# Performance work log

Hardware: AMD Instinct MI355X
Metric: run time of the kernel (lower is better)

Reference implementation:

```python
import jax, jax.numpy as jnp
import numpy as np

B, T, N, E = 16, 30, 2048, 32768
F_IN, HID, TEMP, NCLS = 8, 64, 128, 2
EPS = 1e-5  # BatchNorm eps (eval mode, running stats)


def setup_inputs() -> dict:
    key = jax.random.key(0)
    ks = jax.random.split(key, 26)
    def gl(k, shape, fan_in):
        return (jax.random.normal(k, shape, jnp.float32) / np.sqrt(fan_in)).astype(jnp.float32)
    inp = {}
    inp["x"] = jax.random.normal(ks[0], (B, T, N, F_IN), jnp.float32)
    inp["edge_index"] = jax.random.randint(ks[1], (B, T, 2, E), 0, N)
    inp["edge_weight"] = jax.random.uniform(ks[2], (B, T, E), jnp.float32)
    inp["node_ids"] = jax.random.randint(ks[3], (B, T, N), 0, 1000000)
    # GCN layer 1 and 2 (PyG GCNConv: x @ W then normalized aggregation, + bias)
    inp["W1"] = gl(ks[4], (F_IN, HID), F_IN); inp["b1"] = jnp.zeros((HID,), jnp.float32)
    inp["W2"] = gl(ks[5], (HID, HID), HID);   inp["b2"] = jnp.zeros((HID,), jnp.float32)
    # BatchNorm1d params (eval mode with running stats)
    inp["g1"] = jnp.ones((HID,), jnp.float32); inp["be1"] = jnp.zeros((HID,), jnp.float32)
    inp["m1"] = 0.1 * jax.random.normal(ks[6], (HID,), jnp.float32)
    inp["v1"] = jnp.ones((HID,), jnp.float32) + 0.1 * jax.random.uniform(ks[7], (HID,))
    inp["g2"] = jnp.ones((HID,), jnp.float32); inp["be2"] = jnp.zeros((HID,), jnp.float32)
    inp["m2"] = 0.1 * jax.random.normal(ks[8], (HID,), jnp.float32)
    inp["v2"] = jnp.ones((HID,), jnp.float32) + 0.1 * jax.random.uniform(ks[9], (HID,))
    # GRU (PyTorch layout: W_ih [3*TEMP, HID], W_hh [3*TEMP, TEMP])
    inp["Wih"] = gl(ks[10], (3 * TEMP, HID), HID)
    inp["Whh"] = gl(ks[11], (3 * TEMP, TEMP), TEMP)
    inp["bih"] = jnp.zeros((3 * TEMP,), jnp.float32)
    inp["bhh"] = jnp.zeros((3 * TEMP,), jnp.float32)
    # Classifier MLP: TEMP -> TEMP//2 -> NCLS
    inp["Wc1"] = gl(ks[12], (TEMP, TEMP // 2), TEMP); inp["bc1"] = jnp.zeros((TEMP // 2,), jnp.float32)
    inp["Wc2"] = gl(ks[13], (TEMP // 2, NCLS), TEMP // 2); inp["bc2"] = jnp.zeros((NCLS,), jnp.float32)
    return inp


def _gcn(h, src, dst, ew, W, b):
    # PyG GCNConv with self-loops (weight 1) and symmetric normalization.
    hw = h @ W                                     # [N, out]
    deg = jnp.ones((N,), hw.dtype).at[dst].add(ew)  # in-degree incl. self-loop
    dinv = jnp.where(deg > 0, jax.lax.rsqrt(deg), 0.0)
    norm = dinv[src] * ew * dinv[dst]               # [E]
    agg = jnp.zeros_like(hw).at[dst].add(norm[:, None] * hw[src])
    agg = agg + (dinv * dinv)[:, None] * hw         # self-loop contribution
    return agg + b


def _frame(x, ei, ew, nid, W1, b1, g1, be1, m1, v1, W2, b2, g2, be2, m2, v2):
    # node_ids identity alignment: sort rows of x by node_ids
    x = x[jnp.argsort(nid)]
    src, dst = ei[0], ei[1]
    h = _gcn(x, src, dst, ew, W1, b1)
    h = (h - m1) * jax.lax.rsqrt(v1 + EPS) * g1 + be1  # BN eval
    h = jax.nn.relu(h)
    h = _gcn(h, src, dst, ew, W2, b2)
    h = (h - m2) * jax.lax.rsqrt(v2 + EPS) * g2 + be2
    h = jax.nn.relu(h)
    return h.mean(axis=0)  # frame embedding [HID]


def _forward(x, edge_weight, W1, b1, g1, be1, m1, v1, W2, b2, g2, be2, m2, v2,
             Wih, Whh, bih, bhh, Wc1, bc1, Wc2, bc2, edge_index, node_ids):
    G = B * T
    frames = jax.vmap(
        lambda xf, eif, ewf, nidf: _frame(xf, eif, ewf, nidf, W1, b1, g1, be1,
                                          m1, v1, W2, b2, g2, be2, m2, v2)
    )(x.reshape(G, N, F_IN), edge_index.reshape(G, 2, E),
      edge_weight.reshape(G, E), node_ids.reshape(G, N))
    H = frames.reshape(B, T, HID).transpose(1, 0, 2)  # [T, B, HID]

    def gru_step(h, xt):
        gi = xt @ Wih.T + bih
        gh = h @ Whh.T + bhh
        ir, iz, inn = jnp.split(gi, 3, axis=-1)
        hr, hz, hn = jnp.split(gh, 3, axis=-1)
        r = jax.nn.sigmoid(ir + hr)
        z = jax.nn.sigmoid(iz + hz)
        n = jnp.tanh(inn + r * hn)
        return (1.0 - z) * n + z * h, None

    h0 = jnp.zeros((B, TEMP), H.dtype)
    h_final, _ = jax.lax.scan(gru_step, h0, H)
    hidden = jax.nn.relu(h_final @ Wc1 + bc1)
    return hidden @ Wc2 + bc2  # [B, NCLS]


def reference(x, edge_index, edge_weight, node_ids, W1, b1, W2, b2, g1, be1, m1, v1,
              g2, be2, m2, v2, Wih, Whh, bih, bhh, Wc1, bc1, Wc2, bc2):
    return _forward(x, edge_weight, W1, b1, g1, be1, m1, v1, W2, b2, g2, be2, m2, v2,
                    Wih, Whh, bih, bhh, Wc1, bc1, Wc2, bc2, edge_index, node_ids)
```

## Files before the change

kernel.cpp:

```cpp
#include <hip/hip_runtime.h>
#include <hip/hip_fp16.h>
#include <stdint.h>

#define B_   16
#define T_   30
#define NF   480
#define NN   2048
#define EE   32768
#define EPS  1e-5f

typedef unsigned int u32;
typedef unsigned short u16;
typedef __attribute__((ext_vector_type(8))) short short8;
typedef __attribute__((ext_vector_type(4))) float f32x4;

__device__ __forceinline__ u16 f2bf(float f) {
  u32 u = __float_as_uint(f);
  u32 r = u + 0x7FFFu + ((u >> 16) & 1u);
  return (u16)(r >> 16);
}
__device__ __forceinline__ u32 pack2bf(float a, float b) {
  return (u32)f2bf(a) | ((u32)f2bf(b) << 16);
}
__device__ __forceinline__ float bflo(u32 w) { return __uint_as_float(w << 16); }
__device__ __forceinline__ float bfhi(u32 w) { return __uint_as_float(w & 0xFFFF0000u); }
__device__ __forceinline__ u16 f2h(float f) { return __half_as_ushort(__float2half(f)); }
__device__ __forceinline__ float h2f(u16 h) { return __half2float(__ushort_as_half(h)); }
__device__ __forceinline__ u32 pack2h(float a, float b) {
  return (u32)f2h(a) | ((u32)f2h(b) << 16);
}

#define KP_KEYS 0
#define KP_HIST 8192
#define KP_CUM  9216
#define KP_CUR  10240
#define KP_REC  0
#define KP_DINV 131072
#define KP_CNT  139264
#define KP_PERM 147456
#define KP_RANK 151552
#define KP_OFF  155648
#define KP_LDS  156672

__global__ __launch_bounds__(1024) void kPre(
    const int* __restrict__ ei, const float* __restrict__ ew, const int* __restrict__ nid,
    u32* __restrict__ recG, u32* __restrict__ metaG, float* __restrict__ dv2G,
    u32* __restrict__ offG)
{
  extern __shared__ unsigned char smem[];
  const int g = blockIdx.x, t = threadIdx.x;
  const int*   eig  = ei  + (size_t)g * 2 * EE;
  const float* ewg  = ew  + (size_t)g * EE;
  const int*   nidg = nid + (size_t)g * NN;

  u32*  keys = (u32*)(smem + KP_KEYS);
  u32*  hist = (u32*)(smem + KP_HIST);
  u32*  cum  = (u32*)(smem + KP_CUM);
  u32*  cur  = (u32*)(smem + KP_CUR);
  u32*  rec  = (u32*)(smem + KP_REC);
  float* dinv = (float*)(smem + KP_DINV);
  u32*  cnt  = (u32*)(smem + KP_CNT);
  u16*  perm = (u16*)(smem + KP_PERM);
  u16*  rank = (u16*)(smem + KP_RANK);
  u32*  off  = (u32*)(smem + KP_OFF);

  keys[t]        = ((u32)nidg[t] << 11) | (u32)t;
  keys[t + 1024] = ((u32)nidg[t + 1024] << 11) | (u32)(t + 1024);
  dinv[t] = 1.0f; dinv[t + 1024] = 1.0f;
  cnt[t] = 0u; cnt[t + 1024] = 0u;
  __syncthreads();

  for (int k = 2; k <= NN; k <<= 1) {
    for (int j = k >> 1; j > 0; j >>= 1) {
      int i = ((t & ~(j - 1)) << 1) | (t & (j - 1));
      int l = i | j;
      u32 x = keys[i], y = keys[l];
      bool up = ((i & k) == 0);
      if ((x > y) == up) { keys[i] = y; keys[l] = x; }
      __syncthreads();
    }
  }
  perm[2*t]   = (u16)(keys[2*t] & 2047u);
  perm[2*t+1] = (u16)(keys[2*t+1] & 2047u);

  for (int e = t; e < EE; e += 1024) {
    int d = eig[EE + e];
    atomicAdd(&dinv[d], ewg[e]);
    atomicAdd(&cnt[d], 1u);
  }
  __syncthreads();
  dinv[2*t]   = rsqrtf(dinv[2*t]);
  dinv[2*t+1] = rsqrtf(dinv[2*t+1]);

  if (t < 256) hist[t] = 0u;
  __syncthreads();
  for (int i = t; i < NN; i += 1024) {
    u32 L = cnt[i];
    atomicAdd(&hist[L < 255u ? L : 255u], 1u);
  }
  __syncthreads();
  if (t < 256) cum[t] = hist[t];
  __syncthreads();
  for (int o = 1; o < 256; o <<= 1) {
    u32 v = 0u;
    if (t < 256 && t >= o) v = cum[t - o];
    __syncthreads();
    if (t < 256) cum[t] += v;
    __syncthreads();
  }
  if (t < 256) cur[t] = (u32)NN - cum[t];
  __syncthreads();
  if (t < 256) hist[t] = cur[t];
  __syncthreads();
  for (int o = 1; o < 256; o <<= 1) {
    u32 v = 0u;
    if (t < 256 && t >= o) v = hist[t - o];
    __syncthreads();
    if (t < 256) hist[t] += v;
    __syncthreads();
  }
  if (t < 256) {
    u32 ov = hist[t] - cur[t];
    off[t] = ov;
    offG[(size_t)g * 256 + t] = ov;
  }
  __syncthreads();

  for (int i = t; i < NN; i += 1024) {
    u32 L = cnt[i];
    u32 b = L < 255u ? L : 255u;
    u32 r = atomicAdd(&cur[b], 1u);
    rank[i] = (u16)r;
    metaG[(size_t)g * NN + r] = ((u32)perm[i] << 16) | (L & 0xFFFFu);
    float dv = dinv[i];
    dv2G[(size_t)g * NN + r] = dv * dv;
  }
  __syncthreads();
  cnt[t] = 0u; cnt[t + 1024] = 0u;
  __syncthreads();

  for (int e = t; e < EE; e += 1024) {
    int s = eig[e], d = eig[EE + e];
    float nrm = dinv[s] * ewg[e] * dinv[d];
    u32 k = atomicAdd(&cnt[d], 1u);
    u32 pos = off[k] + (u32)rank[d];
    rec[pos] = ((u32)perm[s] << 11) | (u32)(f2h(nrm) >> 5) | ((u32)f2h(nrm) << 27);
    rec[pos] = ((u32)perm[s] << 16) | (u32)f2h(nrm);
  }
  __syncthreads();

  uint4* rg = (uint4*)(recG + (size_t)g * EE);
  const uint4* rl = (const uint4*)rec;
  for (int i = t; i < EE / 4; i += 1024) rg[i] = rl[i];
}

#define KF_H1   0
#define KF_W1   131072
#define KF_T1   133120
#define KF_OFF  133376
#define KF_LDS  134400

__global__ __launch_bounds__(1024, 4) void kFuse(
    const float* __restrict__ x, const u32* __restrict__ recG,
    const u32* __restrict__ metaG, const float* __restrict__ dv2G,
    const u32* __restrict__ offG,
    const float* __restrict__ W1f, const float* __restrict__ t1f,
    u16* __restrict__ aggOut)
{
  extern __shared__ unsigned char smem[];
  float* xs  = (float*)smem;
  u16*  h1   = (u16*)smem;
  float* W1s = (float*)(smem + KF_W1);
  float* t1s = (float*)(smem + KF_T1);
  u32*  offL = (u32*)(smem + KF_OFF);
  const int g = blockIdx.x, t = threadIdx.x;
  const u32* recf = recG + (size_t)g * EE;

  {
    const float4* xg = (const float4*)(x + (size_t)g * NN * 8);
    for (int i = t; i < NN * 2; i += 1024) ((float4*)xs)[i] = xg[i];
  }
  if (t < 512) W1s[t] = W1f[t];
  if (t < 64) t1s[t] = t1f[t];
  if (t >= 512 && t < 768) offL[t - 512] = offG[(size_t)g * 256 + (t - 512)];

  u32 origA[2], lenA[2]; float dvA[2];
  #pragma unroll
  for (int it = 0; it < 2; ++it) {
    u32 r = (u32)(it * 1024 + t);
    u32 m = metaG[(size_t)g * NN + r];
    origA[it] = m >> 16; lenA[it] = m & 0xFFFFu;
    dvA[it] = dv2G[(size_t)g * NN + r];
  }
  __syncthreads();

  float agg[2][8];
#define P1(RC) { u32 rc_ = (RC); u32 s_ = rc_ >> 16; \
    float nm_ = h2f((u16)(rc_ & 0xFFFFu)); \
    const float4* xp_ = (const float4*)(smem + (size_t)s_ * 32); \
    float4 a_ = xp_[0], b_ = xp_[1]; \
    ac0 += nm_*a_.x; ac1 += nm_*a_.y; ac2 += nm_*a_.z; ac3 += nm_*a_.w; \
    ac4 += nm_*b_.x; ac5 += nm_*b_.y; ac6 += nm_*b_.z; ac7 += nm_*b_.w; }
  #pragma unroll
  for (int it = 0; it < 2; ++it) {
    u32 r = (u32)(it * 1024 + t);
    float ac0=0,ac1=0,ac2=0,ac3=0,ac4=0,ac5=0,ac6=0,ac7=0;
    int len = (int)lenA[it];
    int j = 0;
    for (; j + 4 <= len; j += 4) {
      u32 o0 = offL[j], o1 = offL[j+1], o2 = offL[j+2], o3 = offL[j+3];
      u32 q0 = recf[o0 + r], q1 = recf[o1 + r], q2 = recf[o2 + r], q3 = recf[o3 + r];
      P1(q0) P1(q1) P1(q2) P1(q3)
    }
    for (; j < len; ++j) { P1(recf[offL[j] + r]) }
    {
      const float4* xd = (const float4*)(smem + (size_t)origA[it] * 32);
      float4 a = xd[0], b = xd[1];
      float dv = dvA[it];
      ac0 += dv*a.x; ac1 += dv*a.y; ac2 += dv*a.z; ac3 += dv*a.w;
      ac4 += dv*b.x; ac5 += dv*b.y; ac6 += dv*b.z; ac7 += dv*b.w;
    }
    agg[it][0]=ac0; agg[it][1]=ac1; agg[it][2]=ac2; agg[it][3]=ac3;
    agg[it][4]=ac4; agg[it][5]=ac5; agg[it][6]=ac6; agg[it][7]=ac7;
  }
#undef P1

  for (int p = 0; p < 2; ++p) {
    __syncthreads();

    #pragma unroll
    for (int it = 0; it < 2; ++it) {
      float z[32];
      #pragma unroll
      for (int f = 0; f < 32; ++f) z[f] = t1s[p * 32 + f];
      #pragma unroll
      for (int k = 0; k < 8; ++k) {
        float fk = agg[it][k];
        const float4* wr = (const float4*)(W1s + k * 64 + p * 32);
        #pragma unroll
        for (int q = 0; q < 8; ++q) {
          float4 w = wr[q];
          z[4*q]   += fk * w.x; z[4*q+1] += fk * w.y;
          z[4*q+2] += fk * w.z; z[4*q+3] += fk * w.w;
        }
      }
      u32 orig = origA[it];
      u32 sw = (orig >> 1) & 3u;
      uint4* hp = (uint4*)(h1 + (size_t)orig * 32);
      #pragma unroll
      for (int u = 0; u < 4; ++u) {
        int b = u * 8;
        uint4 v = make_uint4(
          pack2h(fmaxf(z[b],   0.f), fmaxf(z[b+1], 0.f)),
          pack2h(fmaxf(z[b+2], 0.f), fmaxf(z[b+3], 0.f)),
          pack2h(fmaxf(z[b+4], 0.f), fmaxf(z[b+5], 0.f)),
          pack2h(fmaxf(z[b+6], 0.f), fmaxf(z[b+7], 0.f)));
        hp[u ^ sw] = v;
      }
    }
    __syncthreads();

#define ROWACC(SRC, NM, OP) { u32 s_ = (SRC); float nm_ = (NM); \
    u32 sw_ = (s_ >> 1) & 3u; \
    const uint4* rp_ = (const uint4*)(h1 + (size_t)s_ * 32); \
    _Pragma("unroll") \
    for (int u = 0; u < 4; ++u) { \
      uint4 w_ = rp_[u ^ sw_]; \
      int b_ = u * 8; \
      acc[b_+0] OP nm_ * h2f((u16)(w_.x & 0xFFFFu)); \
      acc[b_+1] OP nm_ * h2f((u16)(w_.x >> 16)); \
      acc[b_+2] OP nm_ * h2f((u16)(w_.y & 0xFFFFu)); \
      acc[b_+3] OP nm_ * h2f((u16)(w_.y >> 16)); \
      acc[b_+4] OP nm_ * h2f((u16)(w_.z & 0xFFFFu)); \
      acc[b_+5] OP nm_ * h2f((u16)(w_.z >> 16)); \
      acc[b_+6] OP nm_ * h2f((u16)(w_.w & 0xFFFFu)); \
      acc[b_+7] OP nm_ * h2f((u16)(w_.w >> 16)); \
    } }

    for (int it = 0; it < 2; ++it) {
      u32 r = (u32)(it * 1024 + t);
      float acc[32];
      ROWACC(origA[it], dvA[it], =)
      int len = (int)lenA[it];
      for (int j = 0; j < len; ++j) {
        u32 q = recf[offL[j] + r];
        ROWACC(q >> 16, h2f((u16)(q & 0xFFFFu)), +=)
      }
      #pragma unroll
      for (int u = 0; u < 4; ++u) {
        int b = u * 8;
        uint4 o = make_uint4(
          pack2bf(acc[b],   acc[b+1]), pack2bf(acc[b+2], acc[b+3]),
          pack2bf(acc[b+4], acc[b+5]), pack2bf(acc[b+6], acc[b+7]));
        *((uint4*)aggOut + ((size_t)(g * 8 + p * 4 + u)) * NN + r) = o;
      }
    }
#undef ROWACC
  }
}

__global__ void kW2p(const float* __restrict__ W2, const float* __restrict__ b2,
                     const float* __restrict__ g2, const float* __restrict__ be2,
                     const float* __restrict__ m2, const float* __restrict__ v2,
                     const float* __restrict__ W1, const float* __restrict__ b1,
                     const float* __restrict__ g1, const float* __restrict__ be1,
                     const float* __restrict__ m1, const float* __restrict__ v1,
                     u16* __restrict__ W2bT, float* __restrict__ scG, float* __restrict__ tcG,
                     float* __restrict__ W1f, float* __restrict__ t1f)
{
  const int t = threadIdx.x;
  for (int i = t; i < 4096; i += 256) {
    int f = i >> 6, k = i & 63;
    W2bT[i] = f2bf(W2[k * 64 + f]);
  }
  for (int i = t; i < 512; i += 256) {
    int f = i & 63;
    float sc = g1[f] * rsqrtf(v1[f] + EPS);
    W1f[i] = W1[i] * sc;
  }
  if (t < 64) {
    float sc2 = g2[t] * rsqrtf(v2[t] + EPS);
    scG[t] = sc2;
    tcG[t] = (b2[t] - m2[t]) * sc2 + be2[t];
    float sc1 = g1[t] * rsqrtf(v1[t] + EPS);
    t1f[t] = (b1[t] - m1[t]) * sc1 + be1[t];
  }
}

__global__ __launch_bounds__(512) void kB(
    const u16* __restrict__ agg, const u16* __restrict__ W2bT,
    const float* __restrict__ scG, const float* __restrict__ tcG,
    float* __restrict__ frames)
{
  __shared__ u16 W2s[4096];
  __shared__ float part[8][64];
  const int g = blockIdx.x, tid = threadIdx.x;
  const int l = tid & 63, w = tid >> 6;
  const int lc = l & 15, lg = l >> 4;

  ((uint4*)W2s)[tid] = ((const uint4*)W2bT)[tid];
  __syncthreads();

  short8 bfr[4][2];
  float scv[4], tcv[4];
  #pragma unroll
  for (int ct = 0; ct < 4; ++ct) {
    #pragma unroll
    for (int kt = 0; kt < 2; ++kt)
      bfr[ct][kt] = *(const short8*)(W2s + (ct * 16 + lc) * 64 + kt * 32 + lg * 8);
    scv[ct] = scG[ct * 16 + lc];
    tcv[ct] = tcG[ct * 16 + lc];
  }

  const u16* base = agg + (size_t)g * (8 * NN * 8);
  float fs0 = 0.f, fs1 = 0.f, fs2 = 0.f, fs3 = 0.f;

  for (int rti = 0; rti < 16; ++rti) {
    int arow = (w * 16 + rti) * 16 + lc;
    short8 a0 = *(const short8*)(base + ((size_t)(0 * 4 + lg) * NN + arow) * 8);
    short8 a1 = *(const short8*)(base + ((size_t)(1 * 4 + lg) * NN + arow) * 8);
#define CTILE(CT, FS) { \
    f32x4 acc = {0.f, 0.f, 0.f, 0.f}; \
    acc = __builtin_amdgcn_mfma_f32_16x16x32_bf16(a0, bfr[CT][0], acc, 0, 0, 0); \
    acc = __builtin_amdgcn_mfma_f32_16x16x32_bf16(a1, bfr[CT][1], acc, 0, 0, 0); \
    float s_ = fmaxf(acc[0] * scv[CT] + tcv[CT], 0.f) \
             + fmaxf(acc[1] * scv[CT] + tcv[CT], 0.f) \
             + fmaxf(acc[2] * scv[CT] + tcv[CT], 0.f) \
             + fmaxf(acc[3] * scv[CT] + tcv[CT], 0.f); \
    s_ += __shfl_xor(s_, 16); \
    s_ += __shfl_xor(s_, 32); \
    FS += s_; }
    CTILE(0, fs0) CTILE(1, fs1) CTILE(2, fs2) CTILE(3, fs3)
#undef CTILE
  }
  if (l < 16) {
    part[w][ 0 + l] = fs0;
    part[w][16 + l] = fs1;
    part[w][32 + l] = fs2;
    part[w][48 + l] = fs3;
  }
  __syncthreads();
  if (tid < 64) {
    float s = 0.f;
    #pragma unroll
    for (int q = 0; q < 8; ++q) s += part[q][tid];
    frames[g * 64 + tid] = s * (1.0f / 2048.0f);
  }
}

__global__ __launch_bounds__(384, 2) void kC(
    const float* __restrict__ frames,
    const float* __restrict__ Wih, const float* __restrict__ Whh,
    const float* __restrict__ bih, const float* __restrict__ bhh,
    const float* __restrict__ Wc1, const float* __restrict__ bc1,
    const float* __restrict__ Wc2, const float* __restrict__ bc2,
    float* __restrict__ out)
{
  const int b = blockIdx.x;
  const int j = threadIdx.x;
  __shared__ float xt[64], h[128], GI[384], GH[384], hid[64];
  float wih[64], whh[128];
  const float4* wi4 = (const float4*)(Wih + (size_t)j * 64);
  #pragma unroll
  for (int q = 0; q < 16; ++q) { float4 v = wi4[q]; wih[4*q]=v.x; wih[4*q+1]=v.y; wih[4*q+2]=v.z; wih[4*q+3]=v.w; }
  const float4* wh4 = (const float4*)(Whh + (size_t)j * 128);
  #pragma unroll
  for (int q = 0; q < 32; ++q) { float4 v = wh4[q]; whh[4*q]=v.x; whh[4*q+1]=v.y; whh[4*q+2]=v.z; whh[4*q+3]=v.w; }
  float bi = bih[j], bh = bhh[j];
  if (j < 128) h[j] = 0.f;
  __syncthreads();
  for (int t = 0; t < T_; ++t) {
    if (j < 64) xt[j] = frames[((size_t)b * T_ + t) * 64 + j];
    __syncthreads();
    float gi = bi, gh = bh;
    #pragma unroll
    for (int k = 0; k < 64; ++k) gi += xt[k] * wih[k];
    #pragma unroll
    for (int k = 0; k < 128; ++k) gh += h[k] * whh[k];
    GI[j] = gi; GH[j] = gh;
    __syncthreads();
    if (j < 128) {
      float r = 1.f / (1.f + __expf(-(GI[j] + GH[j])));
      float z = 1.f / (1.f + __expf(-(GI[128 + j] + GH[128 + j])));
      float n = tanhf(GI[256 + j] + r * GH[256 + j]);
      h[j] = (1.f - z) * n + z * h[j];
    }
    __syncthreads();
  }
  if (j < 64) {
    float a = bc1[j];
    #pragma unroll 4
    for (int k = 0; k < 128; ++k) a += h[k] * Wc1[k * 64 + j];
    hid[j] = fmaxf(a, 0.f);
  }
  __syncthreads();
  if (j < 2) {
    float o = bc2[j];
    #pragma unroll
    for (int k = 0; k < 64; ++k) o += hid[k] * Wc2[k * 2 + j];
    out[b * 2 + j] = o;
  }
}

extern "C" void kernel_launch(void* const* d_in, const int* in_sizes, int n_in,
                              void* d_out, int out_size, void* d_ws, size_t ws_size,
                              hipStream_t stream) {
  const float* x   = (const float*)d_in[0];
  const int*   ei  = (const int*)d_in[1];
  const float* ew  = (const float*)d_in[2];
  const int*   nid = (const int*)d_in[3];
  const float* W1  = (const float*)d_in[4];
  const float* b1  = (const float*)d_in[5];
  const float* W2  = (const float*)d_in[6];
  const float* b2  = (const float*)d_in[7];
  const float* g1  = (const float*)d_in[8];
  const float* be1 = (const float*)d_in[9];
  const float* m1  = (const float*)d_in[10];
  const float* v1  = (const float*)d_in[11];
  const float* g2  = (const float*)d_in[12];
  const float* be2 = (const float*)d_in[13];
  const float* m2  = (const float*)d_in[14];
  const float* v2  = (const float*)d_in[15];
  const float* Wih = (const float*)d_in[16];
  const float* Whh = (const float*)d_in[17];
  const float* bih = (const float*)d_in[18];
  const float* bhh = (const float*)d_in[19];
  const float* Wc1 = (const float*)d_in[20];
  const float* bc1 = (const float*)d_in[21];
  const float* Wc2 = (const float*)d_in[22];
  const float* bc2 = (const float*)d_in[23];
  float* out = (float*)d_out;

  const size_t REC_OFF   = 0;
  const size_t PL_OFF    = 62914560;
  const size_t META_OFF  = 188743680;
  const size_t DV2_OFF   = 192675840;
  const size_t OFF_OFF   = 196608000;
  const size_t PREP_OFF  = 197099520;
  const size_t FR_OFF    = 197110528;
  if (ws_size < (size_t)197233408) return;

  u32*   rec   = (u32*)((char*)d_ws + REC_OFF);
  u16*   agg2  = (u16*)((char*)d_ws + PL_OFF);
  u32*   metaG = (u32*)((char*)d_ws + META_OFF);
  float* dv2G  = (float*)((char*)d_ws + DV2_OFF);
  u32*   offG  = (u32*)((char*)d_ws + OFF_OFF);
  u16*   W2bT  = (u16*)((char*)d_ws + PREP_OFF);
  float* scG   = (float*)((char*)d_ws + PREP_OFF + 8192);
  float* tcG   = (float*)((char*)d_ws + PREP_OFF + 8448);
  float* W1f   = (float*)((char*)d_ws + PREP_OFF + 8704);
  float* t1f   = (float*)((char*)d_ws + PREP_OFF + 10752);
  float* frm   = (float*)((char*)d_ws + FR_OFF);

  hipFuncSetAttribute((const void*)kPre,  hipFuncAttributeMaxDynamicSharedMemorySize, KP_LDS);
  hipFuncSetAttribute((const void*)kFuse, hipFuncAttributeMaxDynamicSharedMemorySize, KF_LDS);

  kW2p<<<1, 256, 0, stream>>>(W2, b2, g2, be2, m2, v2,
                              W1, b1, g1, be1, m1, v1,
                              W2bT, scG, tcG, W1f, t1f);
  kPre<<<NF, 1024, KP_LDS, stream>>>(ei, ew, nid, rec, metaG, dv2G, offG);
  kFuse<<<NF, 1024, KF_LDS, stream>>>(x, rec, metaG, dv2G, offG, W1f, t1f, agg2);
  kB<<<NF, 512, 0, stream>>>(agg2, W2bT, scG, tcG, frm);
  kC<<<B_, 384, 0, stream>>>(frm, Wih, Whh, bih, bhh, Wc1, bc1, Wc2, bc2, out);
}
```

Before: 466.9 us.

## Split preprocessing into low-LDS metadata kernel and scatter kernel, fold weight prep

The monolithic preprocessing kernel is split in two. kMeta does the bitonic sort, degree accumulation, histogram and rank, using about 35KB of LDS so more blocks can reside per CU. kScatter builds the edge records in the large LDS buffer. The per-node packed permutation/rank and fp16 dinv are stashed in the not-yet-written aggregation output buffer, so kFuse no longer reads a separate fp32 dv2 array. The single-block weight-prep kernel is folded into block 0 of kMeta to drop one launch. The cost is rereading edge data in a second kernel, an extra launch, and reduced dinv precision from storing it in fp16.

```diff
diff --git a/kernel.cpp b/kernel.cpp
--- a/kernel.cpp
+++ b/kernel.cpp
@@ -22,30 +22,35 @@
 __device__ __forceinline__ u32 pack2bf(float a, float b) {
   return (u32)f2bf(a) | ((u32)f2bf(b) << 16);
 }
-__device__ __forceinline__ float bflo(u32 w) { return __uint_as_float(w << 16); }
-__device__ __forceinline__ float bfhi(u32 w) { return __uint_as_float(w & 0xFFFF0000u); }
 __device__ __forceinline__ u16 f2h(float f) { return __half_as_ushort(__float2half(f)); }
 __device__ __forceinline__ float h2f(u16 h) { return __half2float(__ushort_as_half(h)); }
 __device__ __forceinline__ u32 pack2h(float a, float b) {
   return (u32)f2h(a) | ((u32)f2h(b) << 16);
 }
 
-#define KP_KEYS 0
-#define KP_HIST 8192
-#define KP_CUM  9216
-#define KP_CUR  10240
-#define KP_REC  0
-#define KP_DINV 131072
-#define KP_CNT  139264
-#define KP_PERM 147456
-#define KP_RANK 151552
-#define KP_OFF  155648
-#define KP_LDS  156672
-
-__global__ __launch_bounds__(1024) void kPre(
+#define AGG_FRAME_U16 131072
+#define STASH_DINV_U16 4096
+
+#define KM_KEYS 0
+#define KM_DEG  8192
+#define KM_CNT  16384
+#define KM_PR   24576
+#define KM_HIST 32768
+#define KM_CUM  33792
+#define KM_CUR  34816
+#define KM_LDS  35840
+
+__global__ __launch_bounds__(1024) void kMeta(
     const int* __restrict__ ei, const float* __restrict__ ew, const int* __restrict__ nid,
-    u32* __restrict__ recG, u32* __restrict__ metaG, float* __restrict__ dv2G,
-    u32* __restrict__ offG)
+    u32* __restrict__ metaR, u32* __restrict__ offG, u16* __restrict__ aggStash,
+    const float* __restrict__ W2, const float* __restrict__ b2,
+    const float* __restrict__ g2, const float* __restrict__ be2,
+    const float* __restrict__ m2, const float* __restrict__ v2,
+    const float* __restrict__ W1, const float* __restrict__ b1,
+    const float* __restrict__ g1, const float* __restrict__ be1,
+    const float* __restrict__ m1, const float* __restrict__ v1,
+    u16* __restrict__ W2bT, float* __restrict__ scG, float* __restrict__ tcG,
+    float* __restrict__ W1f, float* __restrict__ t1f)
 {
   extern __shared__ unsigned char smem[];
   const int g = blockIdx.x, t = threadIdx.x;
@@ -53,20 +58,20 @@
   const float* ewg  = ew  + (size_t)g * EE;
   const int*   nidg = nid + (size_t)g * NN;
 
-  u32*  keys = (u32*)(smem + KP_KEYS);
-  u32*  hist = (u32*)(smem + KP_HIST);
-  u32*  cum  = (u32*)(smem + KP_CUM);
-  u32*  cur  = (u32*)(smem + KP_CUR);
-  u32*  rec  = (u32*)(smem + KP_REC);
-  float* dinv = (float*)(smem + KP_DINV);
-  u32*  cnt  = (u32*)(smem + KP_CNT);
-  u16*  perm = (u16*)(smem + KP_PERM);
-  u16*  rank = (u16*)(smem + KP_RANK);
-  u32*  off  = (u32*)(smem + KP_OFF);
+  u32*  keys = (u32*)(smem + KM_KEYS);
+  float* deg = (float*)(smem + KM_DEG);
+  u32*  cnt  = (u32*)(smem + KM_CNT);
+  u32*  pr   = (u32*)(smem + KM_PR);
+  u32*  hist = (u32*)(smem + KM_HIST);
+  u32*  cum  = (u32*)(smem + KM_CUM);
+  u32*  cur  = (u32*)(smem + KM_CUR);
+
+  u32*  npG  = (u32*)(aggStash + (size_t)g * AGG_FRAME_U16);
+  u16*  dvG  = aggStash + (size_t)g * AGG_FRAME_U16 + STASH_DINV_U16;
 
   keys[t]        = ((u32)nidg[t] << 11) | (u32)t;
   keys[t + 1024] = ((u32)nidg[t + 1024] << 11) | (u32)(t + 1024);
-  dinv[t] = 1.0f; dinv[t + 1024] = 1.0f;
+  deg[t] = 1.0f; deg[t + 1024] = 1.0f;
   cnt[t] = 0u; cnt[t + 1024] = 0u;
   __syncthreads();
 
@@ -80,17 +85,19 @@
       __syncthreads();
     }
   }
-  perm[2*t]   = (u16)(keys[2*t] & 2047u);
-  perm[2*t+1] = (u16)(keys[2*t+1] & 2047u);
+  pr[2*t]   = (keys[2*t]   & 2047u) << 16;
+  pr[2*t+1] = (keys[2*t+1] & 2047u) << 16;
 
   for (int e = t; e < EE; e += 1024) {
     int d = eig[EE + e];
-    atomicAdd(&dinv[d], ewg[e]);
+    atomicAdd(&deg[d], ewg[e]);
     atomicAdd(&cnt[d], 1u);
   }
   __syncthreads();
-  dinv[2*t]   = rsqrtf(dinv[2*t]);
-  dinv[2*t+1] = rsqrtf(dinv[2*t+1]);
+  {
+    float d0 = rsqrtf(deg[2*t]), d1 = rsqrtf(deg[2*t+1]);
+    dvG[2*t] = f2h(d0); dvG[2*t+1] = f2h(d1);
+  }
 
   if (t < 256) hist[t] = 0u;
   __syncthreads();
@@ -119,33 +126,78 @@
     if (t < 256) hist[t] += v;
     __syncthreads();
   }
-  if (t < 256) {
-    u32 ov = hist[t] - cur[t];
-    off[t] = ov;
-    offG[(size_t)g * 256 + t] = ov;
-  }
+  if (t < 256) offG[(size_t)g * 256 + t] = hist[t] - cur[t];
   __syncthreads();
 
   for (int i = t; i < NN; i += 1024) {
     u32 L = cnt[i];
     u32 b = L < 255u ? L : 255u;
     u32 r = atomicAdd(&cur[b], 1u);
-    rank[i] = (u16)r;
-    metaG[(size_t)g * NN + r] = ((u32)perm[i] << 16) | (L & 0xFFFFu);
-    float dv = dinv[i];
-    dv2G[(size_t)g * NN + r] = dv * dv;
-  }
-  __syncthreads();
+    pr[i] |= r;
+    metaR[(size_t)g * NN + r] = (pr[i] & 0xFFFF0000u) | (L & 0xFFFFu);
+  }
+  __syncthreads();
+  npG[2*t]   = pr[2*t];
+  npG[2*t+1] = pr[2*t+1];
+
+  if (g == 0) {
+    for (int i = t; i < 4096; i += 1024) {
+      int f = i >> 6, k = i & 63;
+      W2bT[i] = f2bf(W2[k * 64 + f]);
+    }
+    if (t < 512) {
+      int f = t & 63;
+      float sc = g1[f] * rsqrtf(v1[f] + EPS);
+      W1f[t] = W1[t] * sc;
+    }
+    if (t < 64) {
+      float sc2 = g2[t] * rsqrtf(v2[t] + EPS);
+      scG[t] = sc2;
+      tcG[t] = (b2[t] - m2[t]) * sc2 + be2[t];
+      float sc1 = g1[t] * rsqrtf(v1[t] + EPS);
+      t1f[t] = (b1[t] - m1[t]) * sc1 + be1[t];
+    }
+  }
+}
+
+#define KS_REC  0
+#define KS_CNT  131072
+#define KS_PR   139264
+#define KS_DINV 147456
+#define KS_OFF  151552
+#define KS_LDS  152576
+
+__global__ __launch_bounds__(1024) void kScatter(
+    const int* __restrict__ ei, const float* __restrict__ ew,
+    const u32* __restrict__ offG, const u16* __restrict__ aggStash,
+    u32* __restrict__ recG)
+{
+  extern __shared__ unsigned char smem[];
+  const int g = blockIdx.x, t = threadIdx.x;
+  const int*   eig = ei + (size_t)g * 2 * EE;
+  const float* ewg = ew + (size_t)g * EE;
+
+  u32* rec   = (u32*)(smem + KS_REC);
+  u32* cnt   = (u32*)(smem + KS_CNT);
+  u32* prL   = (u32*)(smem + KS_PR);
+  u16* dinvL = (u16*)(smem + KS_DINV);
+  u32* off   = (u32*)(smem + KS_OFF);
+
+  const u32* npG = (const u32*)(aggStash + (size_t)g * AGG_FRAME_U16);
+  const u16* dvG = aggStash + (size_t)g * AGG_FRAME_U16 + STASH_DINV_U16;
+
+  prL[2*t] = npG[2*t]; prL[2*t+1] = npG[2*t+1];
+  dinvL[2*t] = dvG[2*t]; dinvL[2*t+1] = dvG[2*t+1];
   cnt[t] = 0u; cnt[t + 1024] = 0u;
+  if (t < 256) off[t] = offG[(size_t)g * 256 + t];
   __syncthreads();
 
   for (int e = t; e < EE; e += 1024) {
     int s = eig[e], d = eig[EE + e];
-    float nrm = dinv[s] * ewg[e] * dinv[d];
+    float nrm = h2f(dinvL[s]) * ewg[e] * h2f(dinvL[d]);
     u32 k = atomicAdd(&cnt[d], 1u);
-    u32 pos = off[k] + (u32)rank[d];
-    rec[pos] = ((u32)perm[s] << 11) | (u32)(f2h(nrm) >> 5) | ((u32)f2h(nrm) << 27);
-    rec[pos] = ((u32)perm[s] << 16) | (u32)f2h(nrm);
+    u32 pos = off[k] + (prL[d] & 0xFFFFu);
+    rec[pos] = (prL[s] & 0xFFFF0000u) | (u32)f2h(nrm);
   }
   __syncthreads();
 
@@ -160,10 +212,9 @@
 #define KF_OFF  133376
 #define KF_LDS  134400
 
-__global__ __launch_bounds__(1024, 4) void kFuse(
+__global__ __launch_bounds__(1024) void kFuse(
     const float* __restrict__ x, const u32* __restrict__ recG,
-    const u32* __restrict__ metaG, const float* __restrict__ dv2G,
-    const u32* __restrict__ offG,
+    const u32* __restrict__ metaR, const u32* __restrict__ offG,
     const float* __restrict__ W1f, const float* __restrict__ t1f,
     u16* __restrict__ aggOut)
 {
@@ -175,6 +226,7 @@
   u32*  offL = (u32*)(smem + KF_OFF);
   const int g = blockIdx.x, t = threadIdx.x;
   const u32* recf = recG + (size_t)g * EE;
+  const u16* dvN  = aggOut + (size_t)g * AGG_FRAME_U16 + STASH_DINV_U16;
 
   {
     const float4* xg = (const float4*)(x + (size_t)g * NN * 8);
@@ -188,9 +240,10 @@
   #pragma unroll
   for (int it = 0; it < 2; ++it) {
     u32 r = (u32)(it * 1024 + t);
-    u32 m = metaG[(size_t)g * NN + r];
+    u32 m = metaR[(size_t)g * NN + r];
     origA[it] = m >> 16; lenA[it] = m & 0xFFFFu;
-    dvA[it] = dv2G[(size_t)g * NN + r];
+    float dv = h2f(dvN[origA[it]]);
+    dvA[it] = dv * dv;
   }
   __syncthreads();
 
@@ -299,34 +352,6 @@
   }
 }
 
-__global__ void kW2p(const float* __restrict__ W2, const float* __restrict__ b2,
-                     const float* __restrict__ g2, const float* __restrict__ be2,
-                     const float* __restrict__ m2, const float* __restrict__ v2,
-                     const float* __restrict__ W1, const float* __restrict__ b1,
-                     const float* __restrict__ g1, const float* __restrict__ be1,
-                     const float* __restrict__ m1, const float* __restrict__ v1,
-                     u16* __restrict__ W2bT, float* __restrict__ scG, float* __restrict__ tcG,
-                     float* __restrict__ W1f, float* __restrict__ t1f)
-{
-  const int t = threadIdx.x;
-  for (int i = t; i < 4096; i += 256) {
-    int f = i >> 6, k = i & 63;
-    W2bT[i] = f2bf(W2[k * 64 + f]);
-  }
-  for (int i = t; i < 512; i += 256) {
-    int f = i & 63;
-    float sc = g1[f] * rsqrtf(v1[f] + EPS);
-    W1f[i] = W1[i] * sc;
-  }
-  if (t < 64) {
-    float sc2 = g2[t] * rsqrtf(v2[t] + EPS);
-    scG[t] = sc2;
-    tcG[t] = (b2[t] - m2[t]) * sc2 + be2[t];
-    float sc1 = g1[t] * rsqrtf(v1[t] + EPS);
-    t1f[t] = (b1[t] - m1[t]) * sc1 + be1[t];
-  }
-}
-
 __global__ __launch_bounds__(512) void kB(
     const u16* __restrict__ agg, const u16* __restrict__ W2bT,
     const float* __restrict__ scG, const float* __restrict__ tcG,
@@ -479,11 +504,11 @@
   const size_t PREP_OFF  = 197099520;
   const size_t FR_OFF    = 197110528;
   if (ws_size < (size_t)197233408) return;
+  (void)DV2_OFF;
 
   u32*   rec   = (u32*)((char*)d_ws + REC_OFF);
   u16*   agg2  = (u16*)((char*)d_ws + PL_OFF);
-  u32*   metaG = (u32*)((char*)d_ws + META_OFF);
-  float* dv2G  = (float*)((char*)d_ws + DV2_OFF);
+  u32*   metaR = (u32*)((char*)d_ws + META_OFF);
   u32*   offG  = (u32*)((char*)d_ws + OFF_OFF);
   u16*   W2bT  = (u16*)((char*)d_ws + PREP_OFF);
   float* scG   = (float*)((char*)d_ws + PREP_OFF + 8192);
@@ -492,14 +517,16 @@
   float* t1f   = (float*)((char*)d_ws + PREP_OFF + 10752);
   float* frm   = (float*)((char*)d_ws + FR_OFF);
 
-  hipFuncSetAttribute((const void*)kPre,  hipFuncAttributeMaxDynamicSharedMemorySize, KP_LDS);
-  hipFuncSetAttribute((const void*)kFuse, hipFuncAttributeMaxDynamicSharedMemorySize, KF_LDS);
-
-  kW2p<<<1, 256, 0, stream>>>(W2, b2, g2, be2, m2, v2,
-                              W1, b1, g1, be1, m1, v1,
-                              W2bT, scG, tcG, W1f, t1f);
-  kPre<<<NF, 1024, KP_LDS, stream>>>(ei, ew, nid, rec, metaG, dv2G, offG);
-  kFuse<<<NF, 1024, KF_LDS, stream>>>(x, rec, metaG, dv2G, offG, W1f, t1f, agg2);
+  hipFuncSetAttribute((const void*)kMeta,    hipFuncAttributeMaxDynamicSharedMemorySize, KM_LDS);
+  hipFuncSetAttribute((const void*)kScatter, hipFuncAttributeMaxDynamicSharedMemorySize, KS_LDS);
+  hipFuncSetAttribute((const void*)kFuse,    hipFuncAttributeMaxDynamicSharedMemorySize, KF_LDS);
+
+  kMeta<<<NF, 1024, KM_LDS, stream>>>(ei, ew, nid, metaR, offG, agg2,
+                                      W2, b2, g2, be2, m2, v2,
+                                      W1, b1, g1, be1, m1, v1,
+                                      W2bT, scG, tcG, W1f, t1f);
+  kScatter<<<NF, 1024, KS_LDS, stream>>>(ei, ew, offG, agg2, rec);
+  kFuse<<<NF, 1024, KF_LDS, stream>>>(x, rec, metaR, offG, W1f, t1f, agg2);
   kB<<<NF, 512, 0, stream>>>(agg2, W2bT, scG, tcG, frm);
   kC<<<B_, 384, 0, stream>>>(frm, Wih, Whh, bih, bhh, Wc1, bc1, Wc2, bc2, out);
 }
```

New measurement: 462.6 us. No clear change (-0.9%).
